# Optimization experiments

Hardware: AMD Instinct MI355X
Metric: run time of the kernel (lower is better)

## Reference

```python
import jax, jax.numpy as jnp
import numpy as np

EPS = 1e-5
NEG_SLOPE = 0.01  # F.leaky_relu default

N0, N1, N2 = 100000, 25000, 5000
E0, E1 = 800000, 160000
D_IN, D_HID, D_OUT = 256, 256, 128


def setup_inputs() -> dict:
    key = jax.random.key(0)
    ks = jax.random.split(key, 16)
    inp = {
        "x": jax.random.normal(ks[0], (N0, D_IN), dtype=jnp.float32),
        "src0": jax.random.randint(ks[1], (E0,), 0, N0, dtype=jnp.int32),
        "dst0": jax.random.randint(ks[2], (E0,), 0, N1, dtype=jnp.int32),
        "val0": jnp.arange(E0, dtype=jnp.int32),
        "src1": jax.random.randint(ks[3], (E1,), 0, N1, dtype=jnp.int32),
        "dst1": jax.random.randint(ks[4], (E1,), 0, N2, dtype=jnp.int32),
        "val1": jnp.arange(E1, dtype=jnp.int32),
        "timestamps": jax.random.randint(ks[5], (E0 + E1,), 0, 100, dtype=jnp.int32),
        "time": 50,
        "interval": 10,
        # SAGEConv layer 1 (in -> hidden): lin_l (bias) on aggregated, lin_r (no bias) on root
        "W1l": jax.random.normal(ks[6], (D_IN, D_HID), dtype=jnp.float32) / np.sqrt(D_IN),
        "W1r": jax.random.normal(ks[7], (D_IN, D_HID), dtype=jnp.float32) / np.sqrt(D_IN),
        "b1": jnp.zeros((D_HID,), dtype=jnp.float32),
        # BatchNorm1d params (eval mode: running stats)
        "g1": jnp.ones((D_HID,), dtype=jnp.float32),
        "bt1": jnp.zeros((D_HID,), dtype=jnp.float32),
        "rm1": jax.random.normal(ks[8], (D_HID,), dtype=jnp.float32) * 0.1,
        "rv1": jax.random.uniform(ks[9], (D_HID,), dtype=jnp.float32) + 0.5,
        # SAGEConv layer 2 (hidden -> out)
        "W2l": jax.random.normal(ks[10], (D_HID, D_OUT), dtype=jnp.float32) / np.sqrt(D_HID),
        "W2r": jax.random.normal(ks[11], (D_HID, D_OUT), dtype=jnp.float32) / np.sqrt(D_HID),
        "b2": jnp.zeros((D_OUT,), dtype=jnp.float32),
    }
    return inp


def _time_mask(val, timestamps, time, interval):
    # time_sparse keeps edges whose timestamp is in {time, ..., time+interval-1}
    ts = timestamps[val]
    return (ts >= time) & (ts < time + interval)


def _sage_conv(x_src, x_tgt, src, dst, mask, Wl, Wr, b, n_tgt):
    m = mask.astype(x_src.dtype)
    msg = x_src[src] * m[:, None]               # [E, D] gather + mask
    agg = jax.ops.segment_sum(msg, dst, num_segments=n_tgt)
    deg = jax.ops.segment_sum(m, dst, num_segments=n_tgt)
    agg = agg / jnp.maximum(deg, 1.0)[:, None]  # mean aggregation
    return agg @ Wl + b + x_tgt @ Wr


def reference(x, src0, dst0, val0, src1, dst1, val1, timestamps, time, interval,
              W1l, W1r, b1, g1, bt1, rm1, rv1, W2l, W2r, b2):
    # layer 0: N0 -> N1
    mask0 = _time_mask(val0, timestamps, time, interval)
    h = _sage_conv(x, x[:N1], src0, dst0, mask0, W1l, W1r, b1, N1)
    # BatchNorm1d (eval) + leaky_relu; dropout is identity in eval
    h = (h - rm1) * jax.lax.rsqrt(rv1 + EPS) * g1 + bt1
    h = jnp.where(h >= 0, h, NEG_SLOPE * h)
    # layer 1: N1 -> N2
    mask1 = _time_mask(val1, timestamps, time, interval)
    out = _sage_conv(h, h[:N2], src1, dst1, mask1, W2l, W2r, b2, N2)
    return out, mask1
```

## Files before the change

### kernel.cpp

```cpp
#include <hip/hip_runtime.h>

#define N1c 25000
#define N2c 5000
#define Dc 256
#define DOUTc 128
#define EPSc 1e-5f
#define NEGc 0.01f

typedef __attribute__((ext_vector_type(8))) short short8;
typedef __attribute__((ext_vector_type(4))) float f32x4;

__device__ __forceinline__ ushort f2bf(float f) {
    unsigned u = __float_as_uint(f);
    u += 0x7fffu + ((u >> 16) & 1u);
    return (ushort)(u >> 16);
}
__device__ __forceinline__ float bf2f(ushort u) {
    return __uint_as_float(((unsigned)u) << 16);
}

__global__ void mask_out_kernel(const int* __restrict__ val,
                                const int* __restrict__ ts,
                                const int* __restrict__ time_p,
                                const int* __restrict__ itv_p,
                                int E, float* __restrict__ out) {
    int e = blockIdx.x * blockDim.x + threadIdx.x;
    if (e >= E) return;
    int t0 = *time_p, iv = *itv_p;
    int t = ts[val[e]];
    out[e] = (t >= t0 && t < t0 + iv) ? 1.0f : 0.0f;
}

__global__ void count_kernel(const int* __restrict__ dst,
                             const int* __restrict__ val,
                             const int* __restrict__ ts,
                             const int* __restrict__ time_p,
                             const int* __restrict__ itv_p,
                             int E, int* __restrict__ count) {
    int e = blockIdx.x * blockDim.x + threadIdx.x;
    if (e >= E) return;
    int t0 = *time_p, iv = *itv_p;
    int t = ts[val[e]];
    if (t < t0 || t >= t0 + iv) return;
    atomicAdd(&count[dst[e]], 1);
}

template <int CH>
__global__ __launch_bounds__(1024) void scan_kernel(const int* __restrict__ count,
                                                    int* __restrict__ offsets, int n) {
    __shared__ int sums[1024];
    int t = threadIdx.x;
    int v[CH];
    int base = t * CH;
    int run = 0;
#pragma unroll
    for (int i = 0; i < CH; ++i) {
        int idx = base + i;
        int c = (idx < n) ? count[idx] : 0;
        run += c;
        v[i] = run;
    }
    sums[t] = run;
    __syncthreads();
    for (int off = 1; off < 1024; off <<= 1) {
        int x = (t >= off) ? sums[t - off] : 0;
        __syncthreads();
        sums[t] += x;
        __syncthreads();
    }
    int pre = (t == 0) ? 0 : sums[t - 1];
    if (t == 0) offsets[0] = 0;
#pragma unroll
    for (int i = 0; i < CH; ++i) {
        int idx = base + i;
        if (idx < n) offsets[idx + 1] = pre + v[i];
    }
}

__global__ void fill_kernel(const int* __restrict__ src,
                            const int* __restrict__ dst,
                            const int* __restrict__ val,
                            const int* __restrict__ ts,
                            const int* __restrict__ time_p,
                            const int* __restrict__ itv_p,
                            int E,
                            const int* __restrict__ offsets,
                            int* __restrict__ cursor,
                            int* __restrict__ eidx) {
    int e = blockIdx.x * blockDim.x + threadIdx.x;
    if (e >= E) return;
    int t0 = *time_p, iv = *itv_p;
    int t = ts[val[e]];
    if (t < t0 || t >= t0 + iv) return;
    int d = dst[e];
    int pos = atomicAdd(&cursor[d], 1);
    eidx[offsets[d] + pos] = src[e];
}

__global__ void gather_f32(const float* __restrict__ X,
                           const int* __restrict__ off,
                           const int* __restrict__ eidx,
                           ushort* __restrict__ agg, int n) {
    int wave = (blockIdx.x * blockDim.x + threadIdx.x) >> 6;
    int lane = threadIdx.x & 63;
    if (wave >= n) return;
    int s0 = off[wave], s1 = off[wave + 1];
    float4 acc = make_float4(0.f, 0.f, 0.f, 0.f);
    for (int j = s0; j < s1; ++j) {
        int s = eidx[j];
        float4 v = *(const float4*)(X + (size_t)s * Dc + lane * 4);
        acc.x += v.x; acc.y += v.y; acc.z += v.z; acc.w += v.w;
    }
    float inv = 1.0f / fmaxf((float)(s1 - s0), 1.0f);
    ushort4 o;
    o.x = f2bf(acc.x * inv); o.y = f2bf(acc.y * inv);
    o.z = f2bf(acc.z * inv); o.w = f2bf(acc.w * inv);
    *(ushort4*)(agg + (size_t)wave * Dc + lane * 4) = o;
}

__global__ void gather_bf16(const ushort* __restrict__ H,
                            const int* __restrict__ off,
                            const int* __restrict__ eidx,
                            ushort* __restrict__ agg, int n) {
    int wave = (blockIdx.x * blockDim.x + threadIdx.x) >> 6;
    int lane = threadIdx.x & 63;
    if (wave >= n) return;
    int s0 = off[wave], s1 = off[wave + 1];
    float4 acc = make_float4(0.f, 0.f, 0.f, 0.f);
    for (int j = s0; j < s1; ++j) {
        int s = eidx[j];
        ushort4 v = *(const ushort4*)(H + (size_t)s * Dc + lane * 4);
        acc.x += bf2f(v.x); acc.y += bf2f(v.y);
        acc.z += bf2f(v.z); acc.w += bf2f(v.w);
    }
    float inv = 1.0f / fmaxf((float)(s1 - s0), 1.0f);
    ushort4 o;
    o.x = f2bf(acc.x * inv); o.y = f2bf(acc.y * inv);
    o.z = f2bf(acc.z * inv); o.w = f2bf(acc.w * inv);
    *(ushort4*)(agg + (size_t)wave * Dc + lane * 4) = o;
}

__global__ void conv_x_kernel(const float* __restrict__ x,
                              ushort* __restrict__ xb, int n4) {
    int i = blockIdx.x * blockDim.x + threadIdx.x;
    if (i >= n4) return;
    float4 v = ((const float4*)x)[i];
    ushort4 o;
    o.x = f2bf(v.x); o.y = f2bf(v.y); o.z = f2bf(v.z); o.w = f2bf(v.w);
    ((ushort4*)xb)[i] = o;
}

__global__ void prep_b(const float* __restrict__ Wl, const float* __restrict__ Wr,
                       int N, ushort* __restrict__ Bt) {
    int k = blockIdx.x;
    int n = threadIdx.x;
    Bt[(size_t)n * 512 + k]       = f2bf(Wl[(size_t)k * N + n]);
    Bt[(size_t)n * 512 + 256 + k] = f2bf(Wr[(size_t)k * N + n]);
}

template <int VARIANT>
__global__ __launch_bounds__(128) void gemm_mfma(
    const ushort* __restrict__ Alo, const ushort* __restrict__ Ahi,
    const ushort* __restrict__ Bt,
    const float* __restrict__ bias,
    const float* __restrict__ g, const float* __restrict__ bt,
    const float* __restrict__ rm, const float* __restrict__ rv,
    void* __restrict__ Cout, int M) {
    __shared__ ushort As[64][40];
    __shared__ ushort Bs[128][40];
    int tid = threadIdx.x;
    int wave = tid >> 6, lane = tid & 63;
    int quad = lane >> 4, l16 = lane & 15;
    int m0 = blockIdx.y * 64, n0 = blockIdx.x * 128;
    f32x4 acc[2][8] = {};
    int ar = tid >> 1;
    int ak = (tid & 1) * 16;
    int bn = tid;
    for (int k0 = 0; k0 < 512; k0 += 32) {
        const ushort* Ag = (k0 < 256)
            ? (Alo + (size_t)(m0 + ar) * Dc + k0 + ak)
            : (Ahi + (size_t)(m0 + ar) * Dc + (k0 - 256) + ak);
        uint4 a0 = make_uint4(0, 0, 0, 0), a1 = make_uint4(0, 0, 0, 0);
        if (m0 + ar < M) {
            a0 = *(const uint4*)Ag;
            a1 = *(const uint4*)(Ag + 8);
        }
        const ushort* Bg = Bt + (size_t)(n0 + bn) * 512 + k0;
        uint4 b0 = *(const uint4*)(Bg + 0);
        uint4 b1 = *(const uint4*)(Bg + 8);
        uint4 b2 = *(const uint4*)(Bg + 16);
        uint4 b3 = *(const uint4*)(Bg + 24);
        __syncthreads();
        *(uint4*)&As[ar][ak] = a0;
        *(uint4*)&As[ar][ak + 8] = a1;
        *(uint4*)&Bs[bn][0] = b0;
        *(uint4*)&Bs[bn][8] = b1;
        *(uint4*)&Bs[bn][16] = b2;
        *(uint4*)&Bs[bn][24] = b3;
        __syncthreads();
        short8 af0 = *(const short8*)&As[wave * 32 + l16][quad * 8];
        short8 af1 = *(const short8*)&As[wave * 32 + 16 + l16][quad * 8];
#pragma unroll
        for (int j = 0; j < 8; ++j) {
            short8 bf = *(const short8*)&Bs[j * 16 + l16][quad * 8];
            acc[0][j] = __builtin_amdgcn_mfma_f32_16x16x32_bf16(af0, bf, acc[0][j], 0, 0, 0);
            acc[1][j] = __builtin_amdgcn_mfma_f32_16x16x32_bf16(af1, bf, acc[1][j], 0, 0, 0);
        }
    }
#pragma unroll
    for (int grp = 0; grp < 2; ++grp) {
#pragma unroll
        for (int j = 0; j < 8; ++j) {
            int gn = n0 + j * 16 + l16;
            float sc = 1.f, sh = bias[gn];
            if (VARIANT == 0) {
                float s = g[gn] * rsqrtf(rv[gn] + EPSc);
                sh = (bias[gn] - rm[gn]) * s + bt[gn];
                sc = s;
            }
            int gmb = m0 + wave * 32 + grp * 16 + quad * 4;
#pragma unroll
            for (int r = 0; r < 4; ++r) {
                int gm = gmb + r;
                if (gm >= M) continue;
                float v = acc[grp][j][r];
                if (VARIANT == 0) {
                    v = v * sc + sh;
                    v = v >= 0.f ? v : NEGc * v;
                    ((ushort*)Cout)[(size_t)gm * Dc + gn] = f2bf(v);
                } else {
                    ((float*)Cout)[(size_t)gm * DOUTc + gn] = v + sh;
                }
            }
        }
    }
}

extern "C" void kernel_launch(void* const* d_in, const int* in_sizes, int n_in,
                              void* d_out, int out_size, void* d_ws, size_t ws_size,
                              hipStream_t stream) {
    const float* x    = (const float*)d_in[0];
    const int* src0   = (const int*)d_in[1];
    const int* dst0   = (const int*)d_in[2];
    const int* val0   = (const int*)d_in[3];
    const int* src1   = (const int*)d_in[4];
    const int* dst1   = (const int*)d_in[5];
    const int* val1   = (const int*)d_in[6];
    const int* ts     = (const int*)d_in[7];
    const int* time_p = (const int*)d_in[8];
    const int* itv_p  = (const int*)d_in[9];
    const float* W1l  = (const float*)d_in[10];
    const float* W1r  = (const float*)d_in[11];
    const float* b1   = (const float*)d_in[12];
    const float* g1   = (const float*)d_in[13];
    const float* bt1  = (const float*)d_in[14];
    const float* rm1  = (const float*)d_in[15];
    const float* rv1  = (const float*)d_in[16];
    const float* W2l  = (const float*)d_in[17];
    const float* W2r  = (const float*)d_in[18];
    const float* b2   = (const float*)d_in[19];
    int E0 = in_sizes[1];
    int E1 = in_sizes[4];
    float* out = (float*)d_out;

    ushort* agg0 = (ushort*)d_ws;
    ushort* xb   = agg0 + (size_t)N1c * Dc;
    ushort* h    = xb   + (size_t)N1c * Dc;
    ushort* agg1 = h    + (size_t)N1c * Dc;
    ushort* Bt1  = agg1 + (size_t)N2c * Dc;
    ushort* Bt2  = Bt1  + 256 * 512;
    int* ip      = (int*)(Bt2 + 128 * 512);
    int* count0   = ip;            ip += N1c;
    int* cursor0  = ip;            ip += N1c;
    int* count1   = ip;            ip += N2c;
    int* cursor1  = ip;            ip += N2c;
    int* offsets0 = ip;            ip += N1c + 1;
    int* offsets1 = ip;            ip += N2c + 1;
    int* eidx0    = ip;            ip += E0;
    int* eidx1    = ip;            ip += E1;

    hipMemsetAsync(count0, 0, (size_t)(2 * N1c + 2 * N2c) * sizeof(int), stream);

    mask_out_kernel<<<(E1 + 255) / 256, 256, 0, stream>>>(
        val1, ts, time_p, itv_p, E1, out + (size_t)N2c * DOUTc);
    prep_b<<<256, 256, 0, stream>>>(W1l, W1r, 256, Bt1);
    prep_b<<<256, 128, 0, stream>>>(W2l, W2r, 128, Bt2);
    conv_x_kernel<<<(N1c * 64 + 255) / 256, 256, 0, stream>>>(x, xb, N1c * 64);

    count_kernel<<<(E0 + 255) / 256, 256, 0, stream>>>(
        dst0, val0, ts, time_p, itv_p, E0, count0);
    scan_kernel<25><<<1, 1024, 0, stream>>>(count0, offsets0, N1c);
    fill_kernel<<<(E0 + 255) / 256, 256, 0, stream>>>(
        src0, dst0, val0, ts, time_p, itv_p, E0, offsets0, cursor0, eidx0);
    gather_f32<<<(N1c + 3) / 4, 256, 0, stream>>>(x, offsets0, eidx0, agg0, N1c);
    gemm_mfma<0><<<dim3(2, (N1c + 63) / 64), 128, 0, stream>>>(
        agg0, xb, Bt1, b1, g1, bt1, rm1, rv1, h, N1c);

    count_kernel<<<(E1 + 255) / 256, 256, 0, stream>>>(
        dst1, val1, ts, time_p, itv_p, E1, count1);
    scan_kernel<5><<<1, 1024, 0, stream>>>(count1, offsets1, N2c);
    fill_kernel<<<(E1 + 255) / 256, 256, 0, stream>>>(
        src1, dst1, val1, ts, time_p, itv_p, E1, offsets1, cursor1, eidx1);
    gather_bf16<<<(N2c + 3) / 4, 256, 0, stream>>>(h, offsets1, eidx1, agg1, N2c);
    gemm_mfma<1><<<dim3(1, (N2c + 63) / 64), 128, 0, stream>>>(
        agg1, h, Bt2, b2, nullptr, nullptr, nullptr, nullptr, out, N2c);
}
```

Before: 306.2 us.

## Fuse CSR build, conversions and layer-0 gather into one cooperative kernel

Replaces the chain of preprocessing kernels (mask output, weight packing, x conversion, count, scan, fill, layer-0 gather) with one cooperative kernel that uses grid-wide syncs between phases. Both layers' CSR structures are now built together in a single combined count/offset array. The single-block scans become a two-level multi-block scan, and the separate cursor arrays are dropped by atomically advancing the offsets in place. The aim is to cut launch overhead and serial single-block scans. In exchange it runs with only 256 blocks of 256 threads, so the bandwidth-heavy conversion and gather phases get little latency hiding, and each grid sync adds a barrier cost.

```diff
diff --git a/kernel.cpp b/kernel.cpp
--- a/kernel.cpp
+++ b/kernel.cpp
@@ -1,4 +1,7 @@
 #include <hip/hip_runtime.h>
+#include <hip/hip_cooperative_groups.h>
+
+namespace cg = cooperative_groups;
 
 #define N1c 25000
 #define N2c 5000
@@ -6,6 +9,9 @@
 #define DOUTc 128
 #define EPSc 1e-5f
 #define NEGc 0.01f
+#define NTOT (N1c + N2c)
+#define GBLK 256
+#define BTHR 256
 
 typedef __attribute__((ext_vector_type(8))) short short8;
 typedef __attribute__((ext_vector_type(4))) float f32x4;
@@ -19,113 +25,139 @@
     return __uint_as_float(((unsigned)u) << 16);
 }
 
-__global__ void mask_out_kernel(const int* __restrict__ val,
-                                const int* __restrict__ ts,
-                                const int* __restrict__ time_p,
-                                const int* __restrict__ itv_p,
-                                int E, float* __restrict__ out) {
-    int e = blockIdx.x * blockDim.x + threadIdx.x;
-    if (e >= E) return;
-    int t0 = *time_p, iv = *itv_p;
-    int t = ts[val[e]];
-    out[e] = (t >= t0 && t < t0 + iv) ? 1.0f : 0.0f;
-}
-
-__global__ void count_kernel(const int* __restrict__ dst,
-                             const int* __restrict__ val,
-                             const int* __restrict__ ts,
-                             const int* __restrict__ time_p,
-                             const int* __restrict__ itv_p,
-                             int E, int* __restrict__ count) {
-    int e = blockIdx.x * blockDim.x + threadIdx.x;
-    if (e >= E) return;
-    int t0 = *time_p, iv = *itv_p;
-    int t = ts[val[e]];
-    if (t < t0 || t >= t0 + iv) return;
-    atomicAdd(&count[dst[e]], 1);
-}
-
-template <int CH>
-__global__ __launch_bounds__(1024) void scan_kernel(const int* __restrict__ count,
-                                                    int* __restrict__ offsets, int n) {
-    __shared__ int sums[1024];
-    int t = threadIdx.x;
-    int v[CH];
-    int base = t * CH;
-    int run = 0;
-#pragma unroll
-    for (int i = 0; i < CH; ++i) {
-        int idx = base + i;
-        int c = (idx < n) ? count[idx] : 0;
-        run += c;
-        v[i] = run;
-    }
-    sums[t] = run;
+__global__ __launch_bounds__(BTHR) void coopA(
+    const float* __restrict__ x,
+    const int* __restrict__ src0, const int* __restrict__ dst0, const int* __restrict__ val0,
+    const int* __restrict__ src1, const int* __restrict__ dst1, const int* __restrict__ val1,
+    const int* __restrict__ ts, const int* __restrict__ time_p, const int* __restrict__ itv_p,
+    const float* __restrict__ W1l, const float* __restrict__ W1r,
+    const float* __restrict__ W2l, const float* __restrict__ W2r,
+    int E0, int E1,
+    ushort* __restrict__ xb, ushort* __restrict__ Bt1, ushort* __restrict__ Bt2,
+    int* __restrict__ counts, int* __restrict__ offsets,
+    int* __restrict__ partial, int* __restrict__ bpref,
+    int* __restrict__ eidx, ushort* __restrict__ agg0,
+    float* __restrict__ mask_out) {
+    cg::grid_group grid = cg::this_grid();
+    __shared__ int linc[BTHR];
+    __shared__ int pbuf[BTHR];
+    const int tid = threadIdx.x;
+    const int flat = blockIdx.x * BTHR + tid;
+    const int NT = GBLK * BTHR;
+    const int t0 = *time_p, iv = *itv_p;
+
+    for (int i = flat; i < NTOT; i += NT) counts[i] = 0;
+    for (int i = flat; i < 256 * 512; i += NT) {
+        int n = i >> 9, k = i & 511;
+        float v = (k < 256) ? W1l[(size_t)k * 256 + n] : W1r[(size_t)(k - 256) * 256 + n];
+        Bt1[i] = f2bf(v);
+    }
+    for (int i = flat; i < 128 * 512; i += NT) {
+        int n = i >> 9, k = i & 511;
+        float v = (k < 256) ? W2l[(size_t)k * 128 + n] : W2r[(size_t)(k - 256) * 128 + n];
+        Bt2[i] = f2bf(v);
+    }
+    for (int e = flat; e < E1; e += NT) {
+        int t = ts[val1[e]];
+        mask_out[e] = (t >= t0 && t < t0 + iv) ? 1.0f : 0.0f;
+    }
+    __threadfence();
+    grid.sync();
+
+    for (int i = flat; i < N1c * 64; i += NT) {
+        float4 v = ((const float4*)x)[i];
+        ushort4 o;
+        o.x = f2bf(v.x); o.y = f2bf(v.y); o.z = f2bf(v.z); o.w = f2bf(v.w);
+        ((ushort4*)xb)[i] = o;
+    }
+    for (int e = flat; e < E0; e += NT) {
+        int t = ts[val0[e]];
+        if (t >= t0 && t < t0 + iv) atomicAdd(&counts[dst0[e]], 1);
+    }
+    for (int e = flat; e < E1; e += NT) {
+        int t = ts[val1[e]];
+        if (t >= t0 && t < t0 + iv) atomicAdd(&counts[N1c + dst1[e]], 1);
+    }
+    __threadfence();
+    grid.sync();
+
+    int c = (flat < NTOT) ? counts[flat] : 0;
+    linc[tid] = c;
     __syncthreads();
-    for (int off = 1; off < 1024; off <<= 1) {
-        int x = (t >= off) ? sums[t - off] : 0;
-        __syncthreads();
-        sums[t] += x;
-        __syncthreads();
-    }
-    int pre = (t == 0) ? 0 : sums[t - 1];
-    if (t == 0) offsets[0] = 0;
-#pragma unroll
-    for (int i = 0; i < CH; ++i) {
-        int idx = base + i;
-        if (idx < n) offsets[idx + 1] = pre + v[i];
-    }
-}
-
-__global__ void fill_kernel(const int* __restrict__ src,
-                            const int* __restrict__ dst,
-                            const int* __restrict__ val,
-                            const int* __restrict__ ts,
-                            const int* __restrict__ time_p,
-                            const int* __restrict__ itv_p,
-                            int E,
+    for (int off = 1; off < BTHR; off <<= 1) {
+        int v = (tid >= off) ? linc[tid - off] : 0;
+        __syncthreads();
+        linc[tid] += v;
+        __syncthreads();
+    }
+    if (tid == BTHR - 1) partial[blockIdx.x] = linc[tid];
+    __threadfence();
+    grid.sync();
+
+    if (blockIdx.x == 0) {
+        int pv = partial[tid];
+        pbuf[tid] = pv;
+        __syncthreads();
+        for (int off = 1; off < BTHR; off <<= 1) {
+            int v = (tid >= off) ? pbuf[tid - off] : 0;
+            __syncthreads();
+            pbuf[tid] += v;
+            __syncthreads();
+        }
+        bpref[tid] = pbuf[tid] - pv;
+    }
+    __threadfence();
+    grid.sync();
+
+    if (flat < NTOT) offsets[flat] = bpref[blockIdx.x] + linc[tid] - c;
+    __threadfence();
+    grid.sync();
+
+    for (int e = flat; e < E0; e += NT) {
+        int t = ts[val0[e]];
+        if (t >= t0 && t < t0 + iv) {
+            int pos = atomicAdd(&offsets[dst0[e]], 1);
+            eidx[pos] = src0[e];
+        }
+    }
+    for (int e = flat; e < E1; e += NT) {
+        int t = ts[val1[e]];
+        if (t >= t0 && t < t0 + iv) {
+            int pos = atomicAdd(&offsets[N1c + dst1[e]], 1);
+            eidx[pos] = src1[e];
+        }
+    }
+    __threadfence();
+    grid.sync();
+
+    int wave = flat >> 6, lane = flat & 63;
+    int nwaves = NT >> 6;
+    for (int row = wave; row < N1c; row += nwaves) {
+        int s1 = offsets[row];
+        int s0 = row ? offsets[row - 1] : 0;
+        float4 acc = make_float4(0.f, 0.f, 0.f, 0.f);
+        for (int j = s0; j < s1; ++j) {
+            int s = eidx[j];
+            float4 v = *(const float4*)(x + (size_t)s * Dc + lane * 4);
+            acc.x += v.x; acc.y += v.y; acc.z += v.z; acc.w += v.w;
+        }
+        float inv = 1.0f / fmaxf((float)(s1 - s0), 1.0f);
+        ushort4 o;
+        o.x = f2bf(acc.x * inv); o.y = f2bf(acc.y * inv);
+        o.z = f2bf(acc.z * inv); o.w = f2bf(acc.w * inv);
+        *(ushort4*)(agg0 + (size_t)row * Dc + lane * 4) = o;
+    }
+}
+
+__global__ void gather_bf16(const ushort* __restrict__ H,
                             const int* __restrict__ offsets,
-                            int* __restrict__ cursor,
-                            int* __restrict__ eidx) {
-    int e = blockIdx.x * blockDim.x + threadIdx.x;
-    if (e >= E) return;
-    int t0 = *time_p, iv = *itv_p;
-    int t = ts[val[e]];
-    if (t < t0 || t >= t0 + iv) return;
-    int d = dst[e];
-    int pos = atomicAdd(&cursor[d], 1);
-    eidx[offsets[d] + pos] = src[e];
-}
-
-__global__ void gather_f32(const float* __restrict__ X,
-                           const int* __restrict__ off,
-                           const int* __restrict__ eidx,
-                           ushort* __restrict__ agg, int n) {
-    int wave = (blockIdx.x * blockDim.x + threadIdx.x) >> 6;
-    int lane = threadIdx.x & 63;
-    if (wave >= n) return;
-    int s0 = off[wave], s1 = off[wave + 1];
-    float4 acc = make_float4(0.f, 0.f, 0.f, 0.f);
-    for (int j = s0; j < s1; ++j) {
-        int s = eidx[j];
-        float4 v = *(const float4*)(X + (size_t)s * Dc + lane * 4);
-        acc.x += v.x; acc.y += v.y; acc.z += v.z; acc.w += v.w;
-    }
-    float inv = 1.0f / fmaxf((float)(s1 - s0), 1.0f);
-    ushort4 o;
-    o.x = f2bf(acc.x * inv); o.y = f2bf(acc.y * inv);
-    o.z = f2bf(acc.z * inv); o.w = f2bf(acc.w * inv);
-    *(ushort4*)(agg + (size_t)wave * Dc + lane * 4) = o;
-}
-
-__global__ void gather_bf16(const ushort* __restrict__ H,
-                            const int* __restrict__ off,
                             const int* __restrict__ eidx,
                             ushort* __restrict__ agg, int n) {
     int wave = (blockIdx.x * blockDim.x + threadIdx.x) >> 6;
     int lane = threadIdx.x & 63;
     if (wave >= n) return;
-    int s0 = off[wave], s1 = off[wave + 1];
+    int s1 = offsets[N1c + wave];
+    int s0 = offsets[N1c + wave - 1];
     float4 acc = make_float4(0.f, 0.f, 0.f, 0.f);
     for (int j = s0; j < s1; ++j) {
         int s = eidx[j];
@@ -138,24 +170,6 @@
     o.x = f2bf(acc.x * inv); o.y = f2bf(acc.y * inv);
     o.z = f2bf(acc.z * inv); o.w = f2bf(acc.w * inv);
     *(ushort4*)(agg + (size_t)wave * Dc + lane * 4) = o;
-}
-
-__global__ void conv_x_kernel(const float* __restrict__ x,
-                              ushort* __restrict__ xb, int n4) {
-    int i = blockIdx.x * blockDim.x + threadIdx.x;
-    if (i >= n4) return;
-    float4 v = ((const float4*)x)[i];
-    ushort4 o;
-    o.x = f2bf(v.x); o.y = f2bf(v.y); o.z = f2bf(v.z); o.w = f2bf(v.w);
-    ((ushort4*)xb)[i] = o;
-}
-
-__global__ void prep_b(const float* __restrict__ Wl, const float* __restrict__ Wr,
-                       int N, ushort* __restrict__ Bt) {
-    int k = blockIdx.x;
-    int n = threadIdx.x;
-    Bt[(size_t)n * 512 + k]       = f2bf(Wl[(size_t)k * N + n]);
-    Bt[(size_t)n * 512 + 256 + k] = f2bf(Wr[(size_t)k * N + n]);
 }
 
 template <int VARIANT>
@@ -270,38 +284,29 @@
     ushort* Bt1  = agg1 + (size_t)N2c * Dc;
     ushort* Bt2  = Bt1  + 256 * 512;
     int* ip      = (int*)(Bt2 + 128 * 512);
-    int* count0   = ip;            ip += N1c;
-    int* cursor0  = ip;            ip += N1c;
-    int* count1   = ip;            ip += N2c;
-    int* cursor1  = ip;            ip += N2c;
-    int* offsets0 = ip;            ip += N1c + 1;
-    int* offsets1 = ip;            ip += N2c + 1;
-    int* eidx0    = ip;            ip += E0;
-    int* eidx1    = ip;            ip += E1;
-
-    hipMemsetAsync(count0, 0, (size_t)(2 * N1c + 2 * N2c) * sizeof(int), stream);
-
-    mask_out_kernel<<<(E1 + 255) / 256, 256, 0, stream>>>(
-        val1, ts, time_p, itv_p, E1, out + (size_t)N2c * DOUTc);
-    prep_b<<<256, 256, 0, stream>>>(W1l, W1r, 256, Bt1);
-    prep_b<<<256, 128, 0, stream>>>(W2l, W2r, 128, Bt2);
-    conv_x_kernel<<<(N1c * 64 + 255) / 256, 256, 0, stream>>>(x, xb, N1c * 64);
-
-    count_kernel<<<(E0 + 255) / 256, 256, 0, stream>>>(
-        dst0, val0, ts, time_p, itv_p, E0, count0);
-    scan_kernel<25><<<1, 1024, 0, stream>>>(count0, offsets0, N1c);
-    fill_kernel<<<(E0 + 255) / 256, 256, 0, stream>>>(
-        src0, dst0, val0, ts, time_p, itv_p, E0, offsets0, cursor0, eidx0);
-    gather_f32<<<(N1c + 3) / 4, 256, 0, stream>>>(x, offsets0, eidx0, agg0, N1c);
+    int* counts   = ip;            ip += NTOT;
+    int* offsets  = ip;            ip += NTOT;
+    int* partial  = ip;            ip += GBLK;
+    int* bpref    = ip;            ip += GBLK;
+    int* eidx     = ip;            ip += E0 + E1;
+    float* mask_tail = out + (size_t)N2c * DOUTc;
+
+    void* args[] = {
+        (void*)&x, (void*)&src0, (void*)&dst0, (void*)&val0,
+        (void*)&src1, (void*)&dst1, (void*)&val1,
+        (void*)&ts, (void*)&time_p, (void*)&itv_p,
+        (void*)&W1l, (void*)&W1r, (void*)&W2l, (void*)&W2r,
+        (void*)&E0, (void*)&E1,
+        (void*)&xb, (void*)&Bt1, (void*)&Bt2,
+        (void*)&counts, (void*)&offsets, (void*)&partial, (void*)&bpref,
+        (void*)&eidx, (void*)&agg0, (void*)&mask_tail,
+    };
+    hipLaunchCooperativeKernel((const void*)coopA, dim3(GBLK), dim3(BTHR),
+                               args, 0, stream);
+
     gemm_mfma<0><<<dim3(2, (N1c + 63) / 64), 128, 0, stream>>>(
         agg0, xb, Bt1, b1, g1, bt1, rm1, rv1, h, N1c);
-
-    count_kernel<<<(E1 + 255) / 256, 256, 0, stream>>>(
-        dst1, val1, ts, time_p, itv_p, E1, count1);
-    scan_kernel<5><<<1, 1024, 0, stream>>>(count1, offsets1, N2c);
-    fill_kernel<<<(E1 + 255) / 256, 256, 0, stream>>>(
-        src1, dst1, val1, ts, time_p, itv_p, E1, offsets1, cursor1, eidx1);
-    gather_bf16<<<(N2c + 3) / 4, 256, 0, stream>>>(h, offsets1, eidx1, agg1, N2c);
+    gather_bf16<<<(N2c + 3) / 4, 256, 0, stream>>>(h, offsets, eidx, agg1, N2c);
     gemm_mfma<1><<<dim3(1, (N2c + 63) / 64), 128, 0, stream>>>(
         agg1, h, Bt2, b2, nullptr, nullptr, nullptr, nullptr, out, N2c);
 }
```

Result: slower. 671.7 us (+119.4%).

## Fuse preprocessing, scans and CSR fills for both layers into fewer launches

Applied to the files above, without the earlier changes.

Merges weight transposes, x conversion, mask output and both layers' edge counting into one grid-stride kernel. The two scans now run as one two-block launch, and both CSR fills run in one kernel. The fills use exclusive offsets as atomic cursors, so the separate cursor arrays are dropped and the memset shrinks. The gather kernels read the segment range from the shifted offsets. This removes about ten kernel launches and their serialization gaps, but the fused prep kernel runs several memory-bound phases back to back within each thread, with a fixed grid size.

```diff
diff --git a/kernel.cpp b/kernel.cpp
--- a/kernel.cpp
+++ b/kernel.cpp
@@ -19,35 +19,54 @@
     return __uint_as_float(((unsigned)u) << 16);
 }
 
-__global__ void mask_out_kernel(const int* __restrict__ val,
-                                const int* __restrict__ ts,
-                                const int* __restrict__ time_p,
-                                const int* __restrict__ itv_p,
-                                int E, float* __restrict__ out) {
-    int e = blockIdx.x * blockDim.x + threadIdx.x;
-    if (e >= E) return;
-    int t0 = *time_p, iv = *itv_p;
-    int t = ts[val[e]];
-    out[e] = (t >= t0 && t < t0 + iv) ? 1.0f : 0.0f;
-}
-
-__global__ void count_kernel(const int* __restrict__ dst,
-                             const int* __restrict__ val,
-                             const int* __restrict__ ts,
-                             const int* __restrict__ time_p,
-                             const int* __restrict__ itv_p,
-                             int E, int* __restrict__ count) {
-    int e = blockIdx.x * blockDim.x + threadIdx.x;
-    if (e >= E) return;
-    int t0 = *time_p, iv = *itv_p;
-    int t = ts[val[e]];
-    if (t < t0 || t >= t0 + iv) return;
-    atomicAdd(&count[dst[e]], 1);
+__global__ __launch_bounds__(256) void prep_all(
+    const float* __restrict__ x,
+    const int* __restrict__ dst0, const int* __restrict__ val0,
+    const int* __restrict__ dst1, const int* __restrict__ val1,
+    const int* __restrict__ ts, const int* __restrict__ time_p, const int* __restrict__ itv_p,
+    const float* __restrict__ W1l, const float* __restrict__ W1r,
+    const float* __restrict__ W2l, const float* __restrict__ W2r,
+    int E0, int E1,
+    ushort* __restrict__ xb, ushort* __restrict__ Bt1, ushort* __restrict__ Bt2,
+    int* __restrict__ count0, int* __restrict__ count1,
+    float* __restrict__ mask_out) {
+    const int flat = blockIdx.x * blockDim.x + threadIdx.x;
+    const int NT = gridDim.x * blockDim.x;
+    const int t0 = *time_p, iv = *itv_p;
+
+    for (int i = flat; i < 256 * 512; i += NT) {
+        int n = i >> 9, k = i & 511;
+        float v = (k < 256) ? W1l[(size_t)k * 256 + n] : W1r[(size_t)(k - 256) * 256 + n];
+        Bt1[i] = f2bf(v);
+    }
+    for (int i = flat; i < 128 * 512; i += NT) {
+        int n = i >> 9, k = i & 511;
+        float v = (k < 256) ? W2l[(size_t)k * 128 + n] : W2r[(size_t)(k - 256) * 128 + n];
+        Bt2[i] = f2bf(v);
+    }
+    for (int e = flat; e < E1; e += NT) {
+        int t = ts[val1[e]];
+        mask_out[e] = (t >= t0 && t < t0 + iv) ? 1.0f : 0.0f;
+    }
+    for (int i = flat; i < N1c * 64; i += NT) {
+        float4 v = ((const float4*)x)[i];
+        ushort4 o;
+        o.x = f2bf(v.x); o.y = f2bf(v.y); o.z = f2bf(v.z); o.w = f2bf(v.w);
+        ((ushort4*)xb)[i] = o;
+    }
+    for (int e = flat; e < E0; e += NT) {
+        int t = ts[val0[e]];
+        if (t >= t0 && t < t0 + iv) atomicAdd(&count0[dst0[e]], 1);
+    }
+    for (int e = flat; e < E1; e += NT) {
+        int t = ts[val1[e]];
+        if (t >= t0 && t < t0 + iv) atomicAdd(&count1[dst1[e]], 1);
+    }
 }
 
 template <int CH>
-__global__ __launch_bounds__(1024) void scan_kernel(const int* __restrict__ count,
-                                                    int* __restrict__ offsets, int n) {
+__device__ __forceinline__ void scan_block(const int* __restrict__ count,
+                                           int* __restrict__ offsets, int n) {
     __shared__ int sums[1024];
     int t = threadIdx.x;
     int v[CH];
@@ -55,46 +74,56 @@
     int run = 0;
 #pragma unroll
     for (int i = 0; i < CH; ++i) {
-        int idx = base + i;
-        int c = (idx < n) ? count[idx] : 0;
+        int c = (base + i < n) ? count[base + i] : 0;
+        v[i] = run;
         run += c;
-        v[i] = run;
     }
     sums[t] = run;
     __syncthreads();
     for (int off = 1; off < 1024; off <<= 1) {
-        int x = (t >= off) ? sums[t - off] : 0;
+        int s = (t >= off) ? sums[t - off] : 0;
         __syncthreads();
-        sums[t] += x;
+        sums[t] += s;
         __syncthreads();
     }
-    int pre = (t == 0) ? 0 : sums[t - 1];
-    if (t == 0) offsets[0] = 0;
+    int pre = t ? sums[t - 1] : 0;
 #pragma unroll
     for (int i = 0; i < CH; ++i) {
         int idx = base + i;
-        if (idx < n) offsets[idx + 1] = pre + v[i];
-    }
-}
-
-__global__ void fill_kernel(const int* __restrict__ src,
-                            const int* __restrict__ dst,
-                            const int* __restrict__ val,
-                            const int* __restrict__ ts,
-                            const int* __restrict__ time_p,
-                            const int* __restrict__ itv_p,
-                            int E,
-                            const int* __restrict__ offsets,
-                            int* __restrict__ cursor,
-                            int* __restrict__ eidx) {
+        if (idx < n) offsets[idx] = pre + v[i];
+    }
+}
+
+__global__ __launch_bounds__(1024) void scan_both(
+    const int* __restrict__ count0, int* __restrict__ offsets0,
+    const int* __restrict__ count1, int* __restrict__ offsets1) {
+    if (blockIdx.x == 0) scan_block<25>(count0, offsets0, N1c);
+    else                 scan_block<5>(count1, offsets1, N2c);
+}
+
+__global__ __launch_bounds__(256) void fill_both(
+    const int* __restrict__ src0, const int* __restrict__ dst0, const int* __restrict__ val0,
+    const int* __restrict__ src1, const int* __restrict__ dst1, const int* __restrict__ val1,
+    const int* __restrict__ ts, const int* __restrict__ time_p, const int* __restrict__ itv_p,
+    int E0, int E1,
+    int* __restrict__ offsets0, int* __restrict__ offsets1,
+    int* __restrict__ eidx0, int* __restrict__ eidx1) {
     int e = blockIdx.x * blockDim.x + threadIdx.x;
-    if (e >= E) return;
     int t0 = *time_p, iv = *itv_p;
-    int t = ts[val[e]];
-    if (t < t0 || t >= t0 + iv) return;
-    int d = dst[e];
-    int pos = atomicAdd(&cursor[d], 1);
-    eidx[offsets[d] + pos] = src[e];
+    if (e < E0) {
+        int t = ts[val0[e]];
+        if (t >= t0 && t < t0 + iv) {
+            int pos = atomicAdd(&offsets0[dst0[e]], 1);
+            eidx0[pos] = src0[e];
+        }
+    } else if (e < E0 + E1) {
+        int e1 = e - E0;
+        int t = ts[val1[e1]];
+        if (t >= t0 && t < t0 + iv) {
+            int pos = atomicAdd(&offsets1[dst1[e1]], 1);
+            eidx1[pos] = src1[e1];
+        }
+    }
 }
 
 __global__ void gather_f32(const float* __restrict__ X,
@@ -104,7 +133,8 @@
     int wave = (blockIdx.x * blockDim.x + threadIdx.x) >> 6;
     int lane = threadIdx.x & 63;
     if (wave >= n) return;
-    int s0 = off[wave], s1 = off[wave + 1];
+    int s1 = off[wave];
+    int s0 = wave ? off[wave - 1] : 0;
     float4 acc = make_float4(0.f, 0.f, 0.f, 0.f);
     for (int j = s0; j < s1; ++j) {
         int s = eidx[j];
@@ -125,7 +155,8 @@
     int wave = (blockIdx.x * blockDim.x + threadIdx.x) >> 6;
     int lane = threadIdx.x & 63;
     if (wave >= n) return;
-    int s0 = off[wave], s1 = off[wave + 1];
+    int s1 = off[wave];
+    int s0 = wave ? off[wave - 1] : 0;
     float4 acc = make_float4(0.f, 0.f, 0.f, 0.f);
     for (int j = s0; j < s1; ++j) {
         int s = eidx[j];
@@ -138,24 +169,6 @@
     o.x = f2bf(acc.x * inv); o.y = f2bf(acc.y * inv);
     o.z = f2bf(acc.z * inv); o.w = f2bf(acc.w * inv);
     *(ushort4*)(agg + (size_t)wave * Dc + lane * 4) = o;
-}
-
-__global__ void conv_x_kernel(const float* __restrict__ x,
-                              ushort* __restrict__ xb, int n4) {
-    int i = blockIdx.x * blockDim.x + threadIdx.x;
-    if (i >= n4) return;
-    float4 v = ((const float4*)x)[i];
-    ushort4 o;
-    o.x = f2bf(v.x); o.y = f2bf(v.y); o.z = f2bf(v.z); o.w = f2bf(v.w);
-    ((ushort4*)xb)[i] = o;
-}
-
-__global__ void prep_b(const float* __restrict__ Wl, const float* __restrict__ Wr,
-                       int N, ushort* __restrict__ Bt) {
-    int k = blockIdx.x;
-    int n = threadIdx.x;
-    Bt[(size_t)n * 512 + k]       = f2bf(Wl[(size_t)k * N + n]);
-    Bt[(size_t)n * 512 + 256 + k] = f2bf(Wr[(size_t)k * N + n]);
 }
 
 template <int VARIANT>
@@ -271,36 +284,25 @@
     ushort* Bt2  = Bt1  + 256 * 512;
     int* ip      = (int*)(Bt2 + 128 * 512);
     int* count0   = ip;            ip += N1c;
-    int* cursor0  = ip;            ip += N1c;
     int* count1   = ip;            ip += N2c;
-    int* cursor1  = ip;            ip += N2c;
-    int* offsets0 = ip;            ip += N1c + 1;
-    int* offsets1 = ip;            ip += N2c + 1;
+    int* offsets0 = ip;            ip += N1c;
+    int* offsets1 = ip;            ip += N2c;
     int* eidx0    = ip;            ip += E0;
     int* eidx1    = ip;            ip += E1;
-
-    hipMemsetAsync(count0, 0, (size_t)(2 * N1c + 2 * N2c) * sizeof(int), stream);
-
-    mask_out_kernel<<<(E1 + 255) / 256, 256, 0, stream>>>(
-        val1, ts, time_p, itv_p, E1, out + (size_t)N2c * DOUTc);
-    prep_b<<<256, 256, 0, stream>>>(W1l, W1r, 256, Bt1);
-    prep_b<<<256, 128, 0, stream>>>(W2l, W2r, 128, Bt2);
-    conv_x_kernel<<<(N1c * 64 + 255) / 256, 256, 0, stream>>>(x, xb, N1c * 64);
-
-    count_kernel<<<(E0 + 255) / 256, 256, 0, stream>>>(
-        dst0, val0, ts, time_p, itv_p, E0, count0);
-    scan_kernel<25><<<1, 1024, 0, stream>>>(count0, offsets0, N1c);
-    fill_kernel<<<(E0 + 255) / 256, 256, 0, stream>>>(
-        src0, dst0, val0, ts, time_p, itv_p, E0, offsets0, cursor0, eidx0);
+    float* mask_tail = out + (size_t)N2c * DOUTc;
+
+    hipMemsetAsync(count0, 0, (size_t)(N1c + N2c) * sizeof(int), stream);
+
+    prep_all<<<1024, 256, 0, stream>>>(
+        x, dst0, val0, dst1, val1, ts, time_p, itv_p,
+        W1l, W1r, W2l, W2r, E0, E1, xb, Bt1, Bt2, count0, count1, mask_tail);
+    scan_both<<<2, 1024, 0, stream>>>(count0, offsets0, count1, offsets1);
+    fill_both<<<(E0 + E1 + 255) / 256, 256, 0, stream>>>(
+        src0, dst0, val0, src1, dst1, val1, ts, time_p, itv_p,
+        E0, E1, offsets0, offsets1, eidx0, eidx1);
     gather_f32<<<(N1c + 3) / 4, 256, 0, stream>>>(x, offsets0, eidx0, agg0, N1c);
     gemm_mfma<0><<<dim3(2, (N1c + 63) / 64), 128, 0, stream>>>(
         agg0, xb, Bt1, b1, g1, bt1, rm1, rv1, h, N1c);
-
-    count_kernel<<<(E1 + 255) / 256, 256, 0, stream>>>(
-        dst1, val1, ts, time_p, itv_p, E1, count1);
-    scan_kernel<5><<<1, 1024, 0, stream>>>(count1, offsets1, N2c);
-    fill_kernel<<<(E1 + 255) / 256, 256, 0, stream>>>(
-        src1, dst1, val1, ts, time_p, itv_p, E1, offsets1, cursor1, eidx1);
     gather_bf16<<<(N2c + 3) / 4, 256, 0, stream>>>(h, offsets1, eidx1, agg1, N2c);
     gemm_mfma<1><<<dim3(1, (N2c + 63) / 64), 128, 0, stream>>>(
         agg1, h, Bt2, b2, nullptr, nullptr, nullptr, nullptr, out, N2c);
```

After: 287.3 us. 1.07x faster.
